# Performance work log

Measured on AMD Instinct MI355X. Metric: run time of the kernel, lower is better.

Reference implementation:

```python
import jax, jax.numpy as jnp
import numpy as np

B, N, D = 2, 2048, 768
H = 12
HD = D // H
SCALE = HD ** -0.5
EPS = 1e-8


def exp0(v, c):
    # Poincare exponential map at origin: tanh(sqrt(c)||v||) * v / (sqrt(c)||v||)
    sc = jnp.sqrt(c)
    n = jnp.sqrt(jnp.sum(v * v, axis=-1, keepdims=True))
    n = jnp.maximum(n, EPS)
    return jnp.tanh(sc * n) * v / (sc * n)


def log0(x, c):
    # Poincare log map at origin: artanh(sqrt(c)||x||) * x / (sqrt(c)||x||)
    sc = jnp.sqrt(c)
    n = jnp.sqrt(jnp.sum(x * x, axis=-1, keepdims=True))
    n = jnp.maximum(n, EPS)
    t = jnp.clip(sc * n, 0.0, 1.0 - 1e-7)
    return jnp.arctanh(t) * x / (sc * n)


def setup_inputs() -> dict:
    key = jax.random.key(0)
    k1, k2, k3 = jax.random.split(key, 3)
    c0 = 0.1
    x = jax.random.normal(k1, (B, N, D), dtype=jnp.float32)
    # rescale so sqrt(c)*||x|| = 0.5 -> valid points strictly inside the ball
    xn = jnp.sqrt(jnp.sum(x * x, axis=-1, keepdims=True))
    x = x * (0.5 / (np.sqrt(c0) * jnp.maximum(xn, EPS)))
    w_qkv = jax.random.normal(k2, (3 * D, D), dtype=jnp.float32) * (D ** -0.5)
    w_proj = jax.random.normal(k3, (D, D), dtype=jnp.float32) * (D ** -0.5)
    b_proj = jnp.zeros((D,), dtype=jnp.float32)
    curvature = jnp.asarray(c0, dtype=jnp.float32)
    return {"x": x, "w_qkv": w_qkv, "w_proj": w_proj, "b_proj": b_proj,
            "curvature": curvature}


def reference(x, w_qkv, w_proj, b_proj, curvature):
    c = curvature
    v = log0(x, c)                                   # [B,N,D] tangent vectors
    qkv = jnp.einsum('bnd,ed->bne', v, w_qkv)        # [B,N,3D]
    qkv = qkv.reshape(B, N, 3, H, HD).transpose(2, 0, 3, 1, 4)  # [3,B,H,N,HD]
    q, k, v_proj = qkv[0], qkv[1], qkv[2]
    # Map q,k back onto the manifold for the hyperbolic distance score
    qm = exp0(q, c)                                  # [B,H,N,HD]
    km = exp0(k, c)
    q_nsq = jnp.sum(qm * qm, axis=-1)                # [B,H,N]
    k_nsq = jnp.sum(km * km, axis=-1)                # [B,H,N]
    dot = jnp.einsum('bhnd,bhmd->bhnm', qm, km)      # [B,H,N,N]
    # ||q-k||^2 = ||q||^2 + ||k||^2 - 2 q.k  (avoids [B,H,N,N,HD] intermediate)
    diff_sq = jnp.maximum(q_nsq[..., :, None] + k_nsq[..., None, :] - 2.0 * dot, 0.0)
    q_cl = jnp.minimum(q_nsq, 0.99)
    k_cl = jnp.minimum(k_nsq, 0.99)
    denom = (1.0 - q_cl)[..., :, None] * (1.0 - k_cl)[..., None, :] + 1e-8
    inner = jnp.maximum(1.0 + 2.0 * diff_sq / denom, 1.0 + 1e-7)
    distances = jnp.arccosh(inner)                   # [B,H,N,N]
    scores = -distances * SCALE
    attn = jax.nn.softmax(scores, axis=-1)
    out = jnp.einsum('bhnm,bhmd->bhnd', attn, v_proj)
    out = out.transpose(0, 2, 1, 3).reshape(B, N, D)
    v_out = jnp.einsum('bnd,ed->bne', out, w_proj) + b_proj
    return exp0(v_out, c)                            # [B,N,D] on manifold
```

## Files before the change

kernel.cpp:

```cpp
#include <hip/hip_runtime.h>
#include <cmath>

#define ROWS 4096
#define DIM 768
#define QKV_COLS 2304
#define NHEAD 12
#define HEAD_DIM 64
#define SEQ 2048
#define PADK 72

static constexpr float SCALE_F = 0.125f;
static constexpr float EPS_F   = 1e-8f;

typedef __bf16 bfrag __attribute__((ext_vector_type(8)));
typedef float  f32x4 __attribute__((ext_vector_type(4)));

__device__ __forceinline__ float wave_sum64(float v) {
#pragma unroll
  for (int off = 1; off < 64; off <<= 1) v += __shfl_xor(v, off, 64);
  return v;
}

__device__ __forceinline__ unsigned short f2bf(float f) {
  unsigned u = __float_as_uint(f);
  u += 0x7fffu + ((u >> 16) & 1u);
  return (unsigned short)(u >> 16);
}

__device__ __forceinline__ void gl_lds16(const void* g, void* l) {
  __builtin_amdgcn_global_load_lds((const __attribute__((address_space(1))) void*)g,
                                   (__attribute__((address_space(3))) void*)l, 16, 0, 0);
}

__global__ __launch_bounds__(256) void conv_bf16_2(const float* __restrict__ a, int na,
                                                   const float* __restrict__ b, int nb,
                                                   unsigned short* __restrict__ da,
                                                   unsigned short* __restrict__ db) {
  const int i = (blockIdx.x * 256 + threadIdx.x) * 4;
  const float* s;
  unsigned short* d;
  int j;
  if (i < na) { s = a; d = da; j = i; }
  else { j = i - na; if (j >= nb) return; s = b; d = db; }
  const float4 v = *(const float4*)(s + j);
  ushort4 o;
  o.x = f2bf(v.x); o.y = f2bf(v.y); o.z = f2bf(v.z); o.w = f2bf(v.w);
  *(ushort4*)(d + j) = o;
}

__global__ __launch_bounds__(256) void log0_kernel(const float* __restrict__ x,
                                                   const float* __restrict__ cptr,
                                                   unsigned short* __restrict__ vout) {
  const int lane = threadIdx.x & 63;
  const int row  = (blockIdx.x << 2) + (threadIdx.x >> 6);
  const float* xr = x + (size_t)row * DIM;
  unsigned short* vr = vout + (size_t)row * DIM;
  float vals[12];
  float ss = 0.f;
#pragma unroll
  for (int i = 0; i < 12; ++i) {
    float t = xr[lane + (i << 6)];
    vals[i] = t;
    ss += t * t;
  }
  ss = wave_sum64(ss);
  const float sc  = sqrtf(cptr[0]);
  const float n   = fmaxf(sqrtf(ss), EPS_F);
  const float scn = sc * n;
  const float t   = fminf(scn, 1.0f - 1e-7f);
  const float f   = atanhf(t) / scn;
#pragma unroll
  for (int i = 0; i < 12; ++i) vr[lane + (i << 6)] = f2bf(vals[i] * f);
}

__global__ __launch_bounds__(256) void exp0_out_kernel(const float* __restrict__ vin,
                                                       const float* __restrict__ cptr,
                                                       float* __restrict__ outp) {
  const int lane = threadIdx.x & 63;
  const int row  = (blockIdx.x << 2) + (threadIdx.x >> 6);
  const float* vr = vin + (size_t)row * DIM;
  float* orow = outp + (size_t)row * DIM;
  float vals[12];
  float ss = 0.f;
#pragma unroll
  for (int i = 0; i < 12; ++i) {
    float t = vr[lane + (i << 6)];
    vals[i] = t;
    ss += t * t;
  }
  ss = wave_sum64(ss);
  const float sc  = sqrtf(cptr[0]);
  const float n   = fmaxf(sqrtf(ss), EPS_F);
  const float scn = sc * n;
  const float f   = tanhf(scn) / scn;
#pragma unroll
  for (int i = 0; i < 12; ++i) orow[lane + (i << 6)] = vals[i] * f;
}

template<int BM, int BN>
__global__ __launch_bounds__(256) void gemm_nt_dbuf(const unsigned short* __restrict__ A,
                                                    const unsigned short* __restrict__ B,
                                                    float* __restrict__ C,
                                                    int M, int Ncols, int K,
                                                    const float* __restrict__ bias) {
  constexpr int FI = BM / 32;
  constexpr int FJ = BN / 32;
  constexpr int CH = BM / 64;
  __shared__ unsigned short As[2][BM * 32];
  __shared__ unsigned short Bs[2][BN * 32];
  const int tid = threadIdx.x;
  const int w = tid >> 6, lane = tid & 63;
  const int lq = lane & 15, quad = lane >> 4;
  const int wr = w >> 1, wc = w & 1;
  const int row0 = blockIdx.y * BM;
  const int col0 = blockIdx.x * BN;
  const int srow  = lane >> 2;
  const int skoff = (lane & 3) << 3;

  f32x4 acc[FI][FJ];
#pragma unroll
  for (int i = 0; i < FI; ++i)
#pragma unroll
    for (int j = 0; j < FJ; ++j) acc[i][j] = (f32x4){0.f, 0.f, 0.f, 0.f};

  auto pf = [&](int k0, int buf) {
#pragma unroll
    for (int c = 0; c < CH; ++c) {
      const int r = c * 64 + w * 16;
      gl_lds16(A + (size_t)(row0 + r + srow) * K + k0 + skoff, &As[buf][r * 32]);
      gl_lds16(B + (size_t)(col0 + r + srow) * K + k0 + skoff, &Bs[buf][r * 32]);
    }
  };

  pf(0, 0);
  const int NIT = K / 32;
  for (int it = 0; it < NIT; ++it) {
    const int buf = it & 1;
    __syncthreads();
    if (it + 1 < NIT) pf((it + 1) * 32, buf ^ 1);

    bfrag af[FI], bfg[FJ];
#pragma unroll
    for (int i = 0; i < FI; ++i)
      af[i] = *(const bfrag*)&As[buf][(wr * (BM / 2) + i * 16 + lq) * 32 + (quad << 3)];
#pragma unroll
    for (int j = 0; j < FJ; ++j)
      bfg[j] = *(const bfrag*)&Bs[buf][(wc * (BN / 2) + j * 16 + lq) * 32 + (quad << 3)];
#pragma unroll
    for (int i = 0; i < FI; ++i)
#pragma unroll
      for (int j = 0; j < FJ; ++j)
        acc[i][j] = __builtin_amdgcn_mfma_f32_16x16x32_bf16(af[i], bfg[j], acc[i][j], 0, 0, 0);
  }

#pragma unroll
  for (int i = 0; i < FI; ++i) {
    const int crow = row0 + wr * (BM / 2) + i * 16 + (quad << 2);
#pragma unroll
    for (int j = 0; j < FJ; ++j) {
      const int col = col0 + wc * (BN / 2) + j * 16 + lq;
      const float bj = bias ? bias[col] : 0.0f;
      float* cp = C + (size_t)crow * Ncols + col;
#pragma unroll
      for (int r = 0; r < 4; ++r)
        cp[(size_t)r * Ncols] = acc[i][j][r] + bj;
    }
  }
}

__global__ __launch_bounds__(256) void qkv_prep(const float* __restrict__ qkv,
                                                const float* __restrict__ cptr,
                                                unsigned short* __restrict__ qh,
                                                unsigned short* __restrict__ kh,
                                                unsigned short* __restrict__ vth,
                                                float2* __restrict__ qn2,
                                                float2* __restrict__ kn2) {
  const int qt = blockIdx.x, h = blockIdx.y, b = blockIdx.z;
  const int bh = b * NHEAD + h;
  const int tid = threadIdx.x;
  const int w = tid >> 6, lane = tid & 63;
  const float sc = sqrtf(cptr[0]);

  for (int t = 0; t < 32; ++t) {
    const int vv = w * 32 + t;
    const int which = vv & 1;
    const int r = vv >> 1;
    const int n = qt * 64 + r;
    const float v = qkv[((size_t)(b * SEQ + n)) * QKV_COLS + which * DIM + h * HEAD_DIM + lane];
    const float ss = wave_sum64(v * v);
    const float nn = fmaxf(sqrtf(ss), EPS_F);
    const float scn = sc * nn;
    const float f = tanhf(scn) / scn;
    (which ? kh : qh)[((size_t)bh * SEQ + n) * HEAD_DIM + lane] = f2bf(v * f);
    if (lane == 0) {
      const float nrm = ss * f * f;
      (which ? kn2 : qn2)[(size_t)bh * SEQ + n] =
          make_float2(nrm, 1.0f / (1.0f - fminf(nrm, 0.99f)));
    }
  }

  __shared__ unsigned short T[64 * PADK];
  const int r2 = tid >> 2;
  const int c0 = (tid & 3) << 4;
  const float* src = qkv + ((size_t)(b * SEQ + qt * 64 + r2)) * QKV_COLS + 2 * DIM + h * HEAD_DIM + c0;
#pragma unroll
  for (int z = 0; z < 16; z += 4) {
    const float4 v = *(const float4*)(src + z);
    T[(c0 + z + 0) * PADK + r2] = f2bf(v.x);
    T[(c0 + z + 1) * PADK + r2] = f2bf(v.y);
    T[(c0 + z + 2) * PADK + r2] = f2bf(v.z);
    T[(c0 + z + 3) * PADK + r2] = f2bf(v.w);
  }
  __syncthreads();
  const int d  = tid >> 2;
  const int k0 = (tid & 3) << 4;
  unsigned short* dst = vth + ((size_t)bh * HEAD_DIM + d) * SEQ + (size_t)qt * 64 + k0;
  *(uint4*)dst       = *(const uint4*)&T[d * PADK + k0];
  *(uint4*)(dst + 8) = *(const uint4*)&T[d * PADK + k0 + 8];
}

__global__ __launch_bounds__(256) void flash_mfma(const unsigned short* __restrict__ qh,
                                                  const unsigned short* __restrict__ kh,
                                                  const unsigned short* __restrict__ vth,
                                                  const float2* __restrict__ qn2,
                                                  const float2* __restrict__ kn2,
                                                  unsigned short* __restrict__ attn_out) {
  const int qt = blockIdx.x, h = blockIdx.y, b = blockIdx.z;
  const int bh = b * NHEAD + h;
  const int tid = threadIdx.x;
  const int w = tid >> 6, lane = tid & 63;
  const int lq = lane & 15, quad = lane >> 4;

  __shared__ unsigned short Ks[2][64 * 64];
  __shared__ unsigned short Vt[2][64 * 64];
  __shared__ unsigned short Ps[64 * PADK];
  __shared__ float knA[2][64], knB[2][64];
  __shared__ float l_s[64];

  const unsigned short* qbase = qh + ((size_t)bh * SEQ + (size_t)qt * 64) * HEAD_DIM;
  const float2* qnb = qn2 + (size_t)bh * SEQ + (size_t)qt * 64;
  const float2* knb = kn2 + (size_t)bh * SEQ;

  const int srow = tid >> 3, spos = tid & 7;
  const int sB = spos ^ (srow & 7);
  const char* kgsrc = (const char*)(kh + (size_t)bh * SEQ * HEAD_DIM) + (size_t)srow * 128 + sB * 16;
  const char* vgsrc = (const char*)(vth + (size_t)bh * HEAD_DIM * SEQ) + (size_t)srow * 4096 + sB * 16;

  auto prefetch = [&](int kt, int buf) {
    const char* kp = kgsrc + (size_t)kt * 8192;
    const char* vp = vgsrc + (size_t)kt * 128;
    gl_lds16(kp,          (char*)Ks[buf] + w * 1024);
    gl_lds16(kp + 4096,   (char*)Ks[buf] + 4096 + w * 1024);
    gl_lds16(vp,          (char*)Vt[buf] + w * 1024);
    gl_lds16(vp + 131072, (char*)Vt[buf] + 4096 + w * 1024);
    if (tid < 64) {
      const float2 kv = knb[kt * 64 + tid];
      knA[buf][tid] = kv.x;
      knB[buf][tid] = kv.y;
    }
  };

  bfrag aq[2];
#pragma unroll
  for (int khf = 0; khf < 2; ++khf)
    aq[khf] = *(const bfrag*)(qbase + (size_t)(w * 16 + lq) * HEAD_DIM + khf * 32 + quad * 8);

  const float2 qq = qnb[w * 16 + lq];
  const float qnS = qq.x;
  const float rqS = 2.0f * qq.y;

  f32x4 oacc[4];
#pragma unroll
  for (int d = 0; d < 4; ++d) oacc[d] = (f32x4){0.f, 0.f, 0.f, 0.f};
  float l = 0.0f;
  const int swz = lq & 7;

  prefetch(0, 0);
  for (int kt = 0; kt < SEQ / 64; ++kt) {
    const int buf = kt & 1;
    __syncthreads();
    if (kt + 1 < SEQ / 64) prefetch(kt + 1, buf ^ 1);

    f32x4 s[4];
#pragma unroll
    for (int st = 0; st < 4; ++st) s[st] = (f32x4){0.f, 0.f, 0.f, 0.f};
#pragma unroll
    for (int khf = 0; khf < 2; ++khf)
#pragma unroll
      for (int st = 0; st < 4; ++st) {
        const bfrag ak = *(const bfrag*)&Ks[buf][(st * 16 + lq) * 64 + (((khf << 2) + quad) ^ swz) * 8];
        s[st] = __builtin_amdgcn_mfma_f32_16x16x32_bf16(ak, aq[khf], s[st], 0, 0, 0);
      }

#pragma unroll
    for (int st = 0; st < 4; ++st) {
      const f32x4 kna = *(const f32x4*)&knA[buf][st * 16 + quad * 4];
      const f32x4 knr = *(const f32x4*)&knB[buf][st * 16 + quad * 4];
      unsigned u[4];
#pragma unroll
      for (int i = 0; i < 4; ++i) {
        float tt = fmaf(-2.0f, s[st][i], qnS + kna[i]);
        tt = fmaxf(tt, 0.0f);
        const float inner = fmaf(tt, rqS * knr[i], 1.0f);
        const float root = __builtin_amdgcn_sqrtf(fmaf(inner, inner, -1.0f));
        const float wgt = __builtin_amdgcn_exp2f(-0.125f * __builtin_amdgcn_logf(inner + root));
        u[i] = __float_as_uint(wgt);
        l += __uint_as_float(u[i] & 0xffff0000u);
      }
      uint2 pk;
      pk.x = __builtin_amdgcn_perm(u[1], u[0], 0x07060302u);
      pk.y = __builtin_amdgcn_perm(u[3], u[2], 0x07060302u);
      *(uint2*)&Ps[(w * 16 + lq) * PADK + st * 16 + quad * 4] = pk;
    }

#pragma unroll
    for (int khf = 0; khf < 2; ++khf) {
      const bfrag ap = *(const bfrag*)&Ps[(w * 16 + lq) * PADK + khf * 32 + quad * 8];
#pragma unroll
      for (int d = 0; d < 4; ++d) {
        const bfrag bv = *(const bfrag*)&Vt[buf][(d * 16 + lq) * 64 + (((khf << 2) + quad) ^ swz) * 8];
        oacc[d] = __builtin_amdgcn_mfma_f32_16x16x32_bf16(ap, bv, oacc[d], 0, 0, 0);
      }
    }
  }

  l += __shfl_xor(l, 16, 64);
  l += __shfl_xor(l, 32, 64);
  if (quad == 0) l_s[w * 16 + lq] = l;
  float rl4[4];
#pragma unroll
  for (int i = 0; i < 4; ++i) rl4[i] = __builtin_amdgcn_rcpf(l_s[w * 16 + quad * 4 + i]);

  unsigned short* ob = attn_out + ((size_t)b * SEQ + (size_t)qt * 64 + w * 16) * DIM + h * HEAD_DIM;
#pragma unroll
  for (int d = 0; d < 4; ++d)
#pragma unroll
    for (int i = 0; i < 4; ++i)
      ob[(size_t)(quad * 4 + i) * DIM + d * 16 + lq] = f2bf(oacc[d][i] * rl4[i]);
}

extern "C" void kernel_launch(void* const* d_in, const int* in_sizes, int n_in,
                              void* d_out, int out_size, void* d_ws, size_t ws_size,
                              hipStream_t stream) {
  const float* x      = (const float*)d_in[0];
  const float* w_qkv  = (const float*)d_in[1];
  const float* w_proj = (const float*)d_in[2];
  const float* b_proj = (const float*)d_in[3];
  const float* curv   = (const float*)d_in[4];
  float* outp = (float*)d_out;

  float* ws = (float*)d_ws;
  unsigned short* v_tan_bf = (unsigned short*)ws;
  unsigned short* attn_bf  = (unsigned short*)ws;
  float* qkv   = ws + 1572864;
  float* v_out = qkv;
  unsigned short* qh  = (unsigned short*)(qkv + 9437184);
  unsigned short* kh  = qh + 3145728;
  unsigned short* vth = kh + 3145728;
  unsigned short* wqkv_bf  = vth + 3145728;
  unsigned short* wproj_bf = wqkv_bf + 1769472;
  float2* qn2 = (float2*)(wproj_bf + 589824);
  float2* kn2 = qn2 + 49152;

  conv_bf16_2<<<dim3((2359296 / 4 + 255) / 256), dim3(256), 0, stream>>>(
      w_qkv, 1769472, w_proj, 589824, wqkv_bf, wproj_bf);
  log0_kernel<<<dim3(ROWS / 4), dim3(256), 0, stream>>>(x, curv, v_tan_bf);
  gemm_nt_dbuf<128, 128><<<dim3(QKV_COLS / 128, ROWS / 128), dim3(256), 0, stream>>>(
      v_tan_bf, wqkv_bf, qkv, ROWS, QKV_COLS, DIM, nullptr);
  qkv_prep<<<dim3(SEQ / 64, NHEAD, 2), dim3(256), 0, stream>>>(qkv, curv, qh, kh, vth,
                                                               qn2, kn2);
  flash_mfma<<<dim3(SEQ / 64, NHEAD, 2), dim3(256), 0, stream>>>(qh, kh, vth, qn2,
                                                                 kn2, attn_bf);
  gemm_nt_dbuf<64, 64><<<dim3(DIM / 64, ROWS / 64), dim3(256), 0, stream>>>(
      attn_bf, wproj_bf, v_out, ROWS, DIM, DIM, b_proj);
  exp0_out_kernel<<<dim3(ROWS / 4), dim3(256), 0, stream>>>(v_out, curv, outp);
}
```

Baseline: 227.1 us.

## Restructure flash attention to read K/V directly from global with two wave subtiles

```diff
diff --git a/kernel.cpp b/kernel.cpp
--- a/kernel.cpp
+++ b/kernel.cpp
@@ -219,124 +219,144 @@
   *(uint4*)(dst + 8) = *(const uint4*)&T[d * PADK + k0 + 8];
 }
 
-__global__ __launch_bounds__(256) void flash_mfma(const unsigned short* __restrict__ qh,
+__global__ __launch_bounds__(128) void flash_mfma(const unsigned short* __restrict__ qh,
                                                   const unsigned short* __restrict__ kh,
                                                   const unsigned short* __restrict__ vth,
                                                   const float2* __restrict__ qn2,
                                                   const float2* __restrict__ kn2,
                                                   unsigned short* __restrict__ attn_out) {
-  const int qt = blockIdx.x, h = blockIdx.y, b = blockIdx.z;
+  const int flat = blockIdx.x;
+  const int bhid = flat % 24;
+  const int qt   = flat / 24;
+  const int h = bhid % NHEAD, b = bhid / NHEAD;
   const int bh = b * NHEAD + h;
   const int tid = threadIdx.x;
   const int w = tid >> 6, lane = tid & 63;
   const int lq = lane & 15, quad = lane >> 4;
 
-  __shared__ unsigned short Ks[2][64 * 64];
-  __shared__ unsigned short Vt[2][64 * 64];
   __shared__ unsigned short Ps[64 * PADK];
-  __shared__ float knA[2][64], knB[2][64];
-  __shared__ float l_s[64];
-
-  const unsigned short* qbase = qh + ((size_t)bh * SEQ + (size_t)qt * 64) * HEAD_DIM;
-  const float2* qnb = qn2 + (size_t)bh * SEQ + (size_t)qt * 64;
+
+  const unsigned short* khb = kh  + (size_t)bh * SEQ * HEAD_DIM;
+  const unsigned short* vtb = vth + (size_t)bh * HEAD_DIM * SEQ;
   const float2* knb = kn2 + (size_t)bh * SEQ;
-
-  const int srow = tid >> 3, spos = tid & 7;
-  const int sB = spos ^ (srow & 7);
-  const char* kgsrc = (const char*)(kh + (size_t)bh * SEQ * HEAD_DIM) + (size_t)srow * 128 + sB * 16;
-  const char* vgsrc = (const char*)(vth + (size_t)bh * HEAD_DIM * SEQ) + (size_t)srow * 4096 + sB * 16;
-
-  auto prefetch = [&](int kt, int buf) {
-    const char* kp = kgsrc + (size_t)kt * 8192;
-    const char* vp = vgsrc + (size_t)kt * 128;
-    gl_lds16(kp,          (char*)Ks[buf] + w * 1024);
-    gl_lds16(kp + 4096,   (char*)Ks[buf] + 4096 + w * 1024);
-    gl_lds16(vp,          (char*)Vt[buf] + w * 1024);
-    gl_lds16(vp + 131072, (char*)Vt[buf] + 4096 + w * 1024);
-    if (tid < 64) {
-      const float2 kv = knb[kt * 64 + tid];
-      knA[buf][tid] = kv.x;
-      knB[buf][tid] = kv.y;
+  const unsigned short* qbase = qh + ((size_t)bh * SEQ + (size_t)qt * 64 + w * 32) * HEAD_DIM;
+  const float2* qnb = qn2 + (size_t)bh * SEQ + (size_t)qt * 64 + w * 32;
+
+  bfrag aq[2][2];
+#pragma unroll
+  for (int sp = 0; sp < 2; ++sp)
+#pragma unroll
+    for (int khf = 0; khf < 2; ++khf)
+      aq[sp][khf] = *(const bfrag*)(qbase + (size_t)(sp * 16 + lq) * HEAD_DIM + khf * 32 + quad * 8);
+
+  float qn_h[2], qm2[2];
+#pragma unroll
+  for (int sp = 0; sp < 2; ++sp) {
+    const float2 qq = qnb[sp * 16 + lq];
+    qn_h[sp] = -0.5f * qq.x;
+    qm2[sp]  = -4.0f * qq.y;
+  }
+
+  bfrag ones;
+#pragma unroll
+  for (int j = 0; j < 8; ++j) ones[j] = (__bf16)1.0f;
+
+  f32x4 oacc[2][4];
+  f32x4 lacc[2];
+#pragma unroll
+  for (int sp = 0; sp < 2; ++sp) {
+    lacc[sp] = (f32x4){0.f, 0.f, 0.f, 0.f};
+#pragma unroll
+    for (int d = 0; d < 4; ++d) oacc[sp][d] = (f32x4){0.f, 0.f, 0.f, 0.f};
+  }
+
+  for (int kt = 0; kt < SEQ / 64; ++kt) {
+    const int key0 = kt * 64;
+
+    f32x4 kv0[4], kv1[4];
+#pragma unroll
+    for (int st = 0; st < 4; ++st) {
+      const float* kp = (const float*)(knb + key0 + st * 16 + quad * 4);
+      kv0[st] = *(const f32x4*)kp;
+      kv1[st] = *(const f32x4*)(kp + 4);
     }
-  };
-
-  bfrag aq[2];
-#pragma unroll
-  for (int khf = 0; khf < 2; ++khf)
-    aq[khf] = *(const bfrag*)(qbase + (size_t)(w * 16 + lq) * HEAD_DIM + khf * 32 + quad * 8);
-
-  const float2 qq = qnb[w * 16 + lq];
-  const float qnS = qq.x;
-  const float rqS = 2.0f * qq.y;
-
-  f32x4 oacc[4];
-#pragma unroll
-  for (int d = 0; d < 4; ++d) oacc[d] = (f32x4){0.f, 0.f, 0.f, 0.f};
-  float l = 0.0f;
-  const int swz = lq & 7;
-
-  prefetch(0, 0);
-  for (int kt = 0; kt < SEQ / 64; ++kt) {
-    const int buf = kt & 1;
-    __syncthreads();
-    if (kt + 1 < SEQ / 64) prefetch(kt + 1, buf ^ 1);
-
-    f32x4 s[4];
-#pragma unroll
-    for (int st = 0; st < 4; ++st) s[st] = (f32x4){0.f, 0.f, 0.f, 0.f};
+
+    bfrag ak[4][2];
+#pragma unroll
+    for (int st = 0; st < 4; ++st)
+#pragma unroll
+      for (int khf = 0; khf < 2; ++khf)
+        ak[st][khf] = *(const bfrag*)(khb + (size_t)(key0 + st * 16 + lq) * HEAD_DIM + khf * 32 + quad * 8);
+
+    f32x4 s[2][4];
+#pragma unroll
+    for (int sp = 0; sp < 2; ++sp)
+#pragma unroll
+      for (int st = 0; st < 4; ++st)
+        s[sp][st] = (f32x4){fmaf(kv0[st][0], -0.5f, qn_h[sp]),
+                            fmaf(kv0[st][2], -0.5f, qn_h[sp]),
+                            fmaf(kv1[st][0], -0.5f, qn_h[sp]),
+                            fmaf(kv1[st][2], -0.5f, qn_h[sp])};
 #pragma unroll
     for (int khf = 0; khf < 2; ++khf)
 #pragma unroll
+      for (int sp = 0; sp < 2; ++sp)
+#pragma unroll
+        for (int st = 0; st < 4; ++st)
+          s[sp][st] = __builtin_amdgcn_mfma_f32_16x16x32_bf16(ak[st][khf], aq[sp][khf], s[sp][st], 0, 0, 0);
+
+    bfrag bv[2][4];
+#pragma unroll
+    for (int khf = 0; khf < 2; ++khf)
+#pragma unroll
+      for (int d = 0; d < 4; ++d)
+        bv[khf][d] = *(const bfrag*)(vtb + (size_t)(d * 16 + lq) * SEQ + key0 + khf * 32 + quad * 8);
+
+#pragma unroll
+    for (int sp = 0; sp < 2; ++sp)
+#pragma unroll
       for (int st = 0; st < 4; ++st) {
-        const bfrag ak = *(const bfrag*)&Ks[buf][(st * 16 + lq) * 64 + (((khf << 2) + quad) ^ swz) * 8];
-        s[st] = __builtin_amdgcn_mfma_f32_16x16x32_bf16(ak, aq[khf], s[st], 0, 0, 0);
+        const float rc[4] = {kv0[st][1], kv0[st][3], kv1[st][1], kv1[st][3]};
+        unsigned u[4];
+#pragma unroll
+        for (int i = 0; i < 4; ++i) {
+          const float sm = fminf(s[sp][st][i], 0.0f);
+          const float inner = fmaf(sm, qm2[sp] * rc[i], 1.0f);
+          const float root = __builtin_amdgcn_sqrtf(fmaf(inner, inner, -1.0f));
+          const float wgt = __builtin_amdgcn_exp2f(-0.125f * __builtin_amdgcn_logf(inner + root));
+          u[i] = __float_as_uint(wgt);
+        }
+        uint2 pk;
+        pk.x = __builtin_amdgcn_perm(u[1], u[0], 0x07060302u);
+        pk.y = __builtin_amdgcn_perm(u[3], u[2], 0x07060302u);
+        *(uint2*)&Ps[(w * 32 + sp * 16 + lq) * PADK + st * 16 + quad * 4] = pk;
       }
 
 #pragma unroll
-    for (int st = 0; st < 4; ++st) {
-      const f32x4 kna = *(const f32x4*)&knA[buf][st * 16 + quad * 4];
-      const f32x4 knr = *(const f32x4*)&knB[buf][st * 16 + quad * 4];
-      unsigned u[4];
-#pragma unroll
-      for (int i = 0; i < 4; ++i) {
-        float tt = fmaf(-2.0f, s[st][i], qnS + kna[i]);
-        tt = fmaxf(tt, 0.0f);
-        const float inner = fmaf(tt, rqS * knr[i], 1.0f);
-        const float root = __builtin_amdgcn_sqrtf(fmaf(inner, inner, -1.0f));
-        const float wgt = __builtin_amdgcn_exp2f(-0.125f * __builtin_amdgcn_logf(inner + root));
-        u[i] = __float_as_uint(wgt);
-        l += __uint_as_float(u[i] & 0xffff0000u);
+    for (int khf = 0; khf < 2; ++khf)
+#pragma unroll
+      for (int sp = 0; sp < 2; ++sp) {
+        const bfrag ap = *(const bfrag*)&Ps[(w * 32 + sp * 16 + lq) * PADK + khf * 32 + quad * 8];
+        lacc[sp] = __builtin_amdgcn_mfma_f32_16x16x32_bf16(ap, ones, lacc[sp], 0, 0, 0);
+#pragma unroll
+        for (int d = 0; d < 4; ++d)
+          oacc[sp][d] = __builtin_amdgcn_mfma_f32_16x16x32_bf16(ap, bv[khf][d], oacc[sp][d], 0, 0, 0);
       }
-      uint2 pk;
-      pk.x = __builtin_amdgcn_perm(u[1], u[0], 0x07060302u);
-      pk.y = __builtin_amdgcn_perm(u[3], u[2], 0x07060302u);
-      *(uint2*)&Ps[(w * 16 + lq) * PADK + st * 16 + quad * 4] = pk;
-    }
-
-#pragma unroll
-    for (int khf = 0; khf < 2; ++khf) {
-      const bfrag ap = *(const bfrag*)&Ps[(w * 16 + lq) * PADK + khf * 32 + quad * 8];
-#pragma unroll
-      for (int d = 0; d < 4; ++d) {
-        const bfrag bv = *(const bfrag*)&Vt[buf][(d * 16 + lq) * 64 + (((khf << 2) + quad) ^ swz) * 8];
-        oacc[d] = __builtin_amdgcn_mfma_f32_16x16x32_bf16(ap, bv, oacc[d], 0, 0, 0);
-      }
-    }
-  }
-
-  l += __shfl_xor(l, 16, 64);
-  l += __shfl_xor(l, 32, 64);
-  if (quad == 0) l_s[w * 16 + lq] = l;
-  float rl4[4];
-#pragma unroll
-  for (int i = 0; i < 4; ++i) rl4[i] = __builtin_amdgcn_rcpf(l_s[w * 16 + quad * 4 + i]);
-
-  unsigned short* ob = attn_out + ((size_t)b * SEQ + (size_t)qt * 64 + w * 16) * DIM + h * HEAD_DIM;
-#pragma unroll
-  for (int d = 0; d < 4; ++d)
-#pragma unroll
-    for (int i = 0; i < 4; ++i)
-      ob[(size_t)(quad * 4 + i) * DIM + d * 16 + lq] = f2bf(oacc[d][i] * rl4[i]);
+  }
+
+#pragma unroll
+  for (int sp = 0; sp < 2; ++sp) {
+    float rl4[4];
+#pragma unroll
+    for (int i = 0; i < 4; ++i) rl4[i] = __builtin_amdgcn_rcpf(lacc[sp][i]);
+    unsigned short* ob = attn_out +
+        ((size_t)b * SEQ + (size_t)qt * 64 + w * 32 + sp * 16) * DIM + h * HEAD_DIM;
+#pragma unroll
+    for (int d = 0; d < 4; ++d)
+#pragma unroll
+      for (int i = 0; i < 4; ++i)
+        ob[(size_t)(quad * 4 + i) * DIM + d * 16 + lq] = f2bf(oacc[sp][d][i] * rl4[i]);
+  }
 }
 
 extern "C" void kernel_launch(void* const* d_in, const int* in_sizes, int n_in,
@@ -369,8 +389,7 @@
       v_tan_bf, wqkv_bf, qkv, ROWS, QKV_COLS, DIM, nullptr);
   qkv_prep<<<dim3(SEQ / 64, NHEAD, 2), dim3(256), 0, stream>>>(qkv, curv, qh, kh, vth,
                                                                qn2, kn2);
-  flash_mfma<<<dim3(SEQ / 64, NHEAD, 2), dim3(256), 0, stream>>>(qh, kh, vth, qn2,
-                                                                 kn2, attn_bf);
+  flash_mfma<<<dim3(768), dim3(128), 0, stream>>>(qh, kh, vth, qn2, kn2, attn_bf);
   gemm_nt_dbuf<64, 64><<<dim3(DIM / 64, ROWS / 64), dim3(256), 0, stream>>>(
       attn_bf, wproj_bf, v_out, ROWS, DIM, DIM, b_proj);
   exp0_out_kernel<<<dim3(ROWS / 4), dim3(256), 0, stream>>>(v_out, curv, outp);
```

Result: slower. 261.1 us (+15.0%).
